# Kernel tuning notes

Hardware: AMD Instinct MI355X
Metric: run time of the kernel (lower is better)

Reference implementation:

```python
import jax, jax.numpy as jnp
import numpy as np
from jax import lax

G, BS = 8, 32  # group_num, blocksize


def conv(x, w, b=None, stride=1, pad=0):
    out = lax.conv_general_dilated(x, w, (stride, stride), [(pad, pad), (pad, pad)],
                                   dimension_numbers=('NCHW', 'OIHW', 'NCHW'))
    if b is not None:
        out = out + b[None, :, None, None]
    return out


def prelu(x, a):
    return jnp.where(x >= 0, x, a * x)


def reshape_adap(x, bs):
    # faithful vectorized form of My_Reshape_Adap: channel c = co*bs*bs + p*bs + q
    # goes to output[b, co, i*bs+p, j*bs+q]
    B, C, h, w = x.shape
    co = C // (bs * bs)
    return x.reshape(B, co, bs, bs, h, w).transpose(0, 1, 4, 2, 5, 3).reshape(B, co, h * bs, w * bs)


def setup_inputs() -> dict:
    key = jax.random.key(0)
    ks = jax.random.split(key, 24)
    rn = lambda k, shp, s: (jax.random.normal(k, shp, dtype=jnp.float32) * s)
    inp = {
        'x': rn(ks[0], (1, 1, 256, 256), 1.0),
        'sample_w': rn(ks[1], (G, 13, 1, 32, 32), 0.03),
        'up_w': rn(ks[2], (G, 1024, 13, 1, 1), 0.2),
        'up_b': rn(ks[3], (G, 1024), 0.02),
        'h1_w': rn(ks[4], (G, 64, 1, 3, 3), 0.2),
        'h1_b': rn(ks[5], (G, 64), 0.02),
        'h1_a': jnp.full((G,), 0.25, jnp.float32),
        'fus_w': rn(ks[6], (G - 1, 64, 128, 3, 3), 0.03),
        'fus_b': rn(ks[7], (G - 1, 64), 0.02),
        'fus_a': jnp.full((G - 1,), 0.25, jnp.float32),
        't2_w': rn(ks[8], (G, 64, 64, 3, 3), 0.04),
        't2_b': rn(ks[9], (G, 64), 0.02),
        't2_a': jnp.full((G,), 0.25, jnp.float32),
        't3_w': rn(ks[10], (G, 64, 64, 3, 3), 0.04),
        't3_b': rn(ks[11], (G, 64), 0.02),
        't3_a': jnp.full((G,), 0.25, jnp.float32),
        't4_w': rn(ks[12], (G, 64, 64, 3, 3), 0.04),
        't4_b': rn(ks[13], (G, 64), 0.02),
        't4_a': jnp.full((G,), 0.25, jnp.float32),
        't5_w': rn(ks[14], (G, 1, 64, 3, 3), 0.04),
        't5_b': rn(ks[15], (G, 1), 0.02),
    }
    return inp


def reference(x, sample_w, up_w, up_b, h1_w, h1_b, h1_a, fus_w, fus_b, fus_a,
              t2_w, t2_b, t2_a, t3_w, t3_b, t3_a, t4_w, t4_b, t4_a, t5_w, t5_b):
    outs = []
    feature = None
    for m in range(G):
        # SamplingModule: conv(1->13, k=32, s=32, no bias)
        s = conv(x, sample_w[m], stride=BS)
        # HeadBlock: 1x1 upsample (13->1024) + block scatter reshape + conv(1->64)+PReLU
        u = conv(s, up_w[m], up_b[m])
        r = reshape_adap(u, BS)                       # [B,1,H,W]
        h = prelu(conv(r, h1_w[m], h1_b[m], pad=1), h1_a[m])  # [B,64,H,W]
        if m == 0:
            feature = h
        else:
            # Fusion_concate: conv(128->64)+PReLU on channel concat
            cat = jnp.concatenate([feature, h], axis=1)
            feature = prelu(conv(cat, fus_w[m - 1], fus_b[m - 1], pad=1), fus_a[m - 1])
        t = prelu(conv(feature, t2_w[m], t2_b[m], pad=1), t2_a[m])
        t = prelu(conv(t, t3_w[m], t3_b[m], pad=1), t3_a[m])
        t = prelu(conv(t, t4_w[m], t4_b[m], pad=1), t4_a[m])
        outs.append(conv(t, t5_w[m], t5_b[m], pad=1))
    return jnp.stack(outs)  # [G, B, 1, H, W]
```

## Files before the change

### kernel.cpp

```cpp
#include <hip/hip_runtime.h>

constexpr int H = 256, W = 256, NPIX = H * W;
constexpr int PW = 258;
constexpr size_t PLANE = (size_t)PW * PW * 64;

typedef _Float16 half8 __attribute__((ext_vector_type(8)));
typedef _Float16 half4 __attribute__((ext_vector_type(4)));
typedef float    f32x4 __attribute__((ext_vector_type(4)));
typedef float    f32x16 __attribute__((ext_vector_type(16)));

__device__ __forceinline__ void gl16(const _Float16* g, _Float16* l)
{
    __builtin_amdgcn_global_load_lds(
        (const __attribute__((address_space(1))) unsigned int*)g,
        (__attribute__((address_space(3))) unsigned int*)l, 16, 0, 0);
}

__global__ __launch_bounds__(256)
void prep_k(const float* __restrict__ x, const float* __restrict__ sw,
            const float* __restrict__ uw, const float* __restrict__ ub,
            const float* __restrict__ t2w, const float* __restrict__ t3w,
            const float* __restrict__ t4w, const float* __restrict__ fusw,
            _Float16* __restrict__ planes, _Float16* __restrict__ w16,
            float* __restrict__ r_all)
{
    const int b = blockIdx.x, t = threadIdx.x;
    for (int idx = b * 256 + t; idx < 24 * 1028 * 8; idx += 512 * 256) {
        int c = idx & 7, rem = idx >> 3;
        int p = rem / 1028, bb = rem % 1028;
        int gy, gx;
        if (bb < 258)      { gy = 0;            gx = bb; }
        else if (bb < 516) { gy = 257;          gx = bb - 258; }
        else if (bb < 772) { gy = bb - 516 + 1; gx = 0; }
        else               { gy = bb - 772 + 1; gx = 257; }
        f32x4 z = {0.f, 0.f, 0.f, 0.f};
        *(f32x4*)(planes + (size_t)p * PLANE + ((size_t)(gy * PW + gx) * 64) + c * 8) = z;
    }
    for (int idx = b * 256 + t; idx < 38 * 36864; idx += 512 * 256) {
        int blk = idx / 36864, r2 = idx % 36864;
        int e = r2 & 7, co = (r2 >> 3) & 63, hh = (r2 >> 9) & 1, kk = (r2 >> 10) & 3,
            tap = r2 >> 12;
        const float* src; int cin, cib;
        if (blk < 24) {
            int which = blk >> 3, m = blk & 7;
            src = (which == 0 ? t2w : which == 1 ? t3w : t4w) + (size_t)m * 64 * 64 * 9;
            cin = 64; cib = 0;
        } else {
            int f = (blk - 24) >> 1; cib = ((blk - 24) & 1) * 64;
            src = fusw + (size_t)f * 64 * 128 * 9; cin = 128;
        }
        int ci = cib + (kk * 2 + hh) * 8 + e;
        w16[idx] = (_Float16)src[((size_t)co * cin + ci) * 9 + tap];
    }
    {
        int m = b >> 6, ij = b & 63;
        int i = ij >> 3, j = ij & 7;
        __shared__ float s_lds[16];
        if (t < 208) {
            int c = t >> 4, sub = t & 15;
            float acc = 0.f;
            for (int k = sub * 64; k < sub * 64 + 64; ++k) {
                int p = k >> 5, q = k & 31;
                acc += x[(i * 32 + p) * W + (j * 32 + q)] * sw[(m * 13 + c) * 1024 + k];
            }
            #pragma unroll
            for (int off = 8; off; off >>= 1) acc += __shfl_down(acc, off, 16);
            if (sub == 0) s_lds[c] = acc;
        }
        __syncthreads();
        const float* uwm = uw + m * 1024 * 13;
        float* rm = r_all + m * NPIX;
        #pragma unroll
        for (int pi = 0; pi < 4; ++pi) {
            int px = pi * 256 + t;
            int p = px >> 5, q = px & 31;
            int oc = p * 32 + q;
            float acc = ub[m * 1024 + oc];
            #pragma unroll
            for (int c = 0; c < 13; ++c) acc = fmaf(uwm[oc * 13 + c], s_lds[c], acc);
            rm[((i * 32 + p) << 8) + j * 32 + q] = acc;
        }
    }
}

__global__ __launch_bounds__(256)
void h1_k(const float* __restrict__ r_all, const float* __restrict__ w,
          const float* __restrict__ b, const float* __restrict__ a,
          _Float16* __restrict__ f0)
{
    const float* r = r_all;
    const int t = threadIdx.x;
    const int px = t & 63, cog = t >> 6;
    const int y = blockIdx.x >> 2;
    const int x = ((blockIdx.x & 3) << 6) + px;
    float v[9];
    #pragma unroll
    for (int dy = 0; dy < 3; ++dy) {
        int gy = y + dy - 1;
        #pragma unroll
        for (int dx = 0; dx < 3; ++dx) {
            int gx = x + dx - 1;
            v[dy*3+dx] = ((unsigned)gy < 256u && (unsigned)gx < 256u)
                       ? r[(gy << 8) + gx] : 0.f;
        }
    }
    const float slope = a[0];
    _Float16* op = f0 + ((size_t)((y + 1) * PW + (x + 1))) * 64 + cog * 16;
    #pragma unroll
    for (int cg2 = 0; cg2 < 2; ++cg2) {
        half8 o;
        #pragma unroll
        for (int j = 0; j < 8; ++j) {
            int co = cog * 16 + cg2 * 8 + j;
            float acc = b[co];
            #pragma unroll
            for (int k = 0; k < 9; ++k) acc = fmaf(v[k], w[co*9+k], acc);
            acc = acc >= 0.f ? acc : slope * acc;
            o[j] = (_Float16)acc;
        }
        *(half8*)(op + cg2 * 8) = o;
    }
}

__global__ __launch_bounds__(128, 2)
void conv_mfma_k(const _Float16* __restrict__ in0, const _Float16* __restrict__ w0,
                 const float* __restrict__ bias, const float* __restrict__ alpha,
                 _Float16* __restrict__ out)
{
    const int t    = threadIdx.x;
    const int lane = t & 63;
    const int wv   = t >> 6;
    const int b    = blockIdx.x;
    const int m    = b >> 7;
    const int rem  = b & 127;
    const int xq   = rem & 3;
    const int y0   = (rem >> 2) << 3;
    const int x0   = xq << 6;

    const _Float16* inp0 = in0 + (size_t)m * PLANE;
    _Float16*       outp = out + (size_t)m * PLANE;
    const _Float16* wp0  = w0 + (size_t)m * 36864;
    const float*    bp   = bias + m * 64;
    const float     slope = alpha[m];

    const int h = lane >> 5, cl = lane & 31;
    const int cobase = wv * 32;

    extern __shared__ __align__(16) char smem[];
    _Float16* li = (_Float16*)smem;

    half8 Areg[36];
    #pragma unroll
    for (int tap = 0; tap < 9; ++tap)
        #pragma unroll
        for (int kk = 0; kk < 4; ++kk)
            Areg[tap*4+kk] = *(const half8*)(wp0 +
                (size_t)(((tap*4+kk)*2 + h)*64 + cobase + cl) * 8);

    auto stage_row = [&](int pr) {
        const int slot = pr & 3;
        #pragma unroll
        for (int i = 0; i < 5; ++i) {
            int f = i * 128 + t;
            if (i < 4 || f < 528) {
                int hx = f >> 3, c = f & 7;
                gl16(inp0 + ((size_t)(pr * PW + x0 + hx) * 64 + (c ^ (hx & 7)) * 8),
                     li + (size_t)(slot * 528 + f) * 8);
            }
        }
    };

    f32x16 acc0, acc1;

    stage_row(y0); stage_row(y0 + 1); stage_row(y0 + 2);
    __syncthreads();
    #pragma unroll 1
    for (int s = 0; s < 8; ++s) {
        if (s < 7) stage_row(y0 + s + 3);
        #pragma unroll
        for (int q = 0; q < 4; ++q)
            #pragma unroll
            for (int j = 0; j < 4; ++j) {
                float bb = bp[cobase + q * 8 + 4 * h + j];
                acc0[q*4+j] = bb; acc1[q*4+j] = bb;
            }
        __builtin_amdgcn_s_setprio(1);
        #pragma unroll
        for (int tap = 0; tap < 9; ++tap) {
            const int dy = tap / 3, dx = tap % 3;
            const int slot = (y0 + s + dy) & 3;
            const int hx0 = cl + dx;
            const int hx1 = hx0 + 32;
            const int sw8 = hx0 & 7;
            #pragma unroll
            for (int kk = 0; kk < 4; ++kk) {
                const int c = kk * 2 + h;
                half8 b0 = *(const half8*)(li + ((size_t)(slot*528 + hx0*8 + (c ^ sw8))) * 8);
                half8 b1 = *(const half8*)(li + ((size_t)(slot*528 + hx1*8 + (c ^ sw8))) * 8);
                acc0 = __builtin_amdgcn_mfma_f32_32x32x16_f16(Areg[tap*4+kk], b0, acc0, 0, 0, 0);
                acc1 = __builtin_amdgcn_mfma_f32_32x32x16_f16(Areg[tap*4+kk], b1, acc1, 0, 0, 0);
            }
        }
        __builtin_amdgcn_s_setprio(0);
        const int y = y0 + s;
        #pragma unroll
        for (int pt = 0; pt < 2; ++pt) {
            const size_t gp = (size_t)((y + 1) * PW + (x0 + pt * 32 + cl + 1)) * 64;
            const f32x16& A0 = pt ? acc1 : acc0;
            #pragma unroll
            for (int q = 0; q < 4; ++q) {
                half4 v0;
                #pragma unroll
                for (int j = 0; j < 4; ++j) {
                    float xv = A0[q*4+j];
                    xv = xv >= 0.f ? xv : slope * xv;
                    v0[j] = (_Float16)v0[j];
                    v0[j] = (_Float16)xv;
                }
                *(half4*)(outp + gp + cobase + q * 8 + 4 * h) = v0;
            }
        }
        if (s < 7) {
            asm volatile("s_waitcnt vmcnt(8)" ::: "memory");
            __builtin_amdgcn_s_barrier();
            __builtin_amdgcn_sched_barrier(0);
        }
    }
}

__global__ __launch_bounds__(256, 2)
void fus_k(const _Float16* __restrict__ fprev, const float* __restrict__ rm,
           const float* __restrict__ h1w, const float* __restrict__ h1b,
           const float* __restrict__ h1a,
           const _Float16* __restrict__ wf, const _Float16* __restrict__ wh,
           const float* __restrict__ bias, const float* __restrict__ alpha,
           _Float16* __restrict__ outp)
{
    const int t = threadIdx.x, lane = t & 63, wv = t >> 6;
    const int b = blockIdx.x;
    const int xcd = b & 7, u = b >> 3, xq = u & 3, band = u >> 2;
    const int y0 = xcd * 32 + band * 2, x0 = xq * 64;
    const int h = lane >> 5, cl = lane & 31;
    const int px0 = (wv & 1) * 32, cobase = (wv >> 1) * 32;

    __shared__ __align__(16) _Float16 ringF[4 * 528 * 8];
    __shared__ __align__(16) _Float16 ringH[4 * 528 * 8];

    #pragma unroll
    for (int i = 0; i < 9; ++i) {
        int idx = i * 256 + t;
        if (i < 8 || idx < 2112) {
            int r = idx / 528, f = idx - r * 528;
            int hx = f >> 3, c = f & 7;
            gl16(fprev + ((size_t)((y0 + r) * PW + x0 + hx) * 64 + (c ^ (hx & 7)) * 8),
                 ringF + (size_t)idx * 8);
        }
    }
    {
        const int c8 = t & 7;
        float wreg[72];
        #pragma unroll
        for (int i = 0; i < 18; ++i)
            *(f32x4*)(wreg + i * 4) = *(const f32x4*)(h1w + c8 * 72 + i * 4);
        float b8[8];
        #pragma unroll
        for (int j = 0; j < 8; ++j) b8[j] = h1b[c8 * 8 + j];
        const float hs = h1a[0];

        #pragma unroll
        for (int it = 0; it < 9; ++it) {
            int idx = it * 256 + t;
            if (it < 8 || idx < 2112) {
                int pl = idx >> 3;
                int r  = pl / 66, hx = pl - r * 66;
                int gy = y0 - 1 + r, gx = x0 - 1 + hx;
                half8 o = {0,0,0,0,0,0,0,0};
                if ((unsigned)gy < 256u && (unsigned)gx < 256u) {
                    float v[9];
                    #pragma unroll
                    for (int dy = 0; dy < 3; ++dy) {
                        int ry = gy + dy - 1;
                        #pragma unroll
                        for (int dx = 0; dx < 3; ++dx) {
                            int rx = gx + dx - 1;
                            v[dy*3+dx] = ((unsigned)ry < 256u && (unsigned)rx < 256u)
                                       ? rm[(ry << 8) + rx] : 0.f;
                        }
                    }
                    #pragma unroll
                    for (int j = 0; j < 8; ++j) {
                        float av = b8[j];
                        #pragma unroll
                        for (int k = 0; k < 9; ++k) av = fmaf(v[k], wreg[j*9+k], av);
                        av = av >= 0.f ? av : hs * av;
                        o[j] = (_Float16)av;
                    }
                }
                *(half8*)(ringH + (size_t)(r * 528 + hx * 8 + (c8 ^ (hx & 7))) * 8) = o;
            }
        }
    }
    __builtin_amdgcn_sched_barrier(0);

    half8 Areg[36];
    auto load_A = [&](const _Float16* w) {
        #pragma unroll
        for (int tap = 0; tap < 9; ++tap)
            #pragma unroll
            for (int kk = 0; kk < 4; ++kk)
                Areg[tap*4+kk] = *(const half8*)(w +
                    (size_t)(((tap*4+kk)*2 + h)*64 + cobase + cl) * 8);
    };
    load_A(wf);

    f32x16 acc0, acc1;
    #pragma unroll
    for (int q = 0; q < 4; ++q)
        #pragma unroll
        for (int j = 0; j < 4; ++j) {
            float bb = bias[cobase + q * 8 + 4 * h + j];
            acc0[q*4+j] = bb; acc1[q*4+j] = bb;
        }

    __syncthreads();

    auto cpass = [&](const _Float16* ring) {
        __builtin_amdgcn_s_setprio(1);
        #pragma unroll
        for (int tap = 0; tap < 9; ++tap) {
            const int dy = tap / 3, dx = tap % 3;
            const int hx = px0 + cl + dx;
            const int sw = hx & 7;
            #pragma unroll
            for (int kk = 0; kk < 4; ++kk) {
                const int c = kk * 2 + h;
                half8 b0 = *(const half8*)(ring + ((size_t)(((dy    )*528) + hx*8 + (c ^ sw))) * 8);
                half8 b1 = *(const half8*)(ring + ((size_t)(((dy + 1)*528) + hx*8 + (c ^ sw))) * 8);
                acc0 = __builtin_amdgcn_mfma_f32_32x32x16_f16(Areg[tap*4+kk], b0, acc0, 0, 0, 0);
                acc1 = __builtin_amdgcn_mfma_f32_32x32x16_f16(Areg[tap*4+kk], b1, acc1, 0, 0, 0);
            }
        }
        __builtin_amdgcn_s_setprio(0);
    };

    cpass(ringF);
    load_A(wh);
    cpass(ringH);

    const float slope = alpha[0];
    #pragma unroll
    for (int s = 0; s < 2; ++s) {
        const size_t gp = (size_t)((y0 + s + 1) * PW + (x0 + px0 + cl + 1)) * 64 + cobase;
        const f32x16& A0 = s ? acc1 : acc0;
        #pragma unroll
        for (int q = 0; q < 4; ++q) {
            half4 v;
            #pragma unroll
            for (int j = 0; j < 4; ++j) {
                float xv = A0[q*4+j];
                xv = xv >= 0.f ? xv : slope * xv;
                v[j] = (_Float16)xv;
            }
            *(half4*)(outp + gp + q * 8 + 4 * h) = v;
        }
    }
}

__global__ __launch_bounds__(256, 2)
void t5_k(const _Float16* __restrict__ in_all, const float* __restrict__ w_all,
          const float* __restrict__ b_all, float* __restrict__ out_all)
{
    const int m = blockIdx.y;
    const _Float16* in = in_all + (size_t)m * PLANE;
    const float* w = w_all + m * 576;
    float* outp = out_all + m * NPIX;

    const int t = threadIdx.x;
    const int b = blockIdx.x;
    const int xcd = b & 7, u = b >> 3;
    const int xh = u & 1, band = u >> 1;
    const int y0 = xcd * 32 + band * 8;
    const int x0 = xh << 7;

    __shared__ __align__(16) _Float16 ring[4 * 130 * 64];
    __shared__ float wl[576];
    __shared__ float part[128];

    auto stage_row = [&](int pr) {
        const int slot = pr & 3;
        #pragma unroll
        for (int i = 0; i < 5; ++i) {
            int f = i * 256 + t;
            if (i < 4 || f < 1040) {
                int hx = f >> 3, c = f & 7;
                gl16(in + ((size_t)(pr * PW + x0 + hx) * 64 + (c ^ (hx & 7)) * 8),
                     ring + (size_t)(slot * 1040 + f) * 8);
            }
        }
    };

    stage_row(y0); stage_row(y0 + 1); stage_row(y0 + 2);
    #pragma unroll
    for (int i = 0; i < 3; ++i) { int idx = i*256 + t; if (idx < 576) wl[idx] = w[idx]; }
    __syncthreads();

    const int p = t & 127, chalf = t >> 7;
    #pragma unroll 1
    for (int s = 0; s < 8; ++s) {
        if (s < 7) stage_row(y0 + s + 3);
        float acc = 0.f;
        #pragma unroll
        for (int dy = 0; dy < 3; ++dy) {
            const int slot = (y0 + s + dy) & 3;
            #pragma unroll
            for (int dx = 0; dx < 3; ++dx) {
                const int hx = p + dx, sw = hx & 7, tap = dy * 3 + dx;
                #pragma unroll
                for (int kc = 0; kc < 4; ++kc) {
                    const int c8 = chalf * 4 + kc;
                    half8 vv = *(const half8*)(ring +
                        ((size_t)((slot*130 + hx)*8 + (c8 ^ sw))) * 8);
                    #pragma unroll
                    for (int e = 0; e < 8; ++e)
                        acc = fmaf((float)vv[e], wl[(c8 * 8 + e) * 9 + tap], acc);
                }
            }
        }
        if (chalf) part[p] = acc;
        __syncthreads();
        if (!chalf) outp[((y0 + s) << 8) + x0 + p] = part[p] + acc + b_all[m];
        __syncthreads();
    }
}

extern "C" void kernel_launch(void* const* d_in, const int* in_sizes, int n_in,
                              void* d_out, int out_size, void* d_ws, size_t ws_size,
                              hipStream_t stream)
{
    const float* x        = (const float*)d_in[0];
    const float* sample_w = (const float*)d_in[1];
    const float* up_w     = (const float*)d_in[2];
    const float* up_b     = (const float*)d_in[3];
    const float* h1_w     = (const float*)d_in[4];
    const float* h1_b     = (const float*)d_in[5];
    const float* h1_a     = (const float*)d_in[6];
    const float* fus_w    = (const float*)d_in[7];
    const float* fus_b    = (const float*)d_in[8];
    const float* fus_a    = (const float*)d_in[9];
    const float* t2_w     = (const float*)d_in[10];
    const float* t2_b     = (const float*)d_in[11];
    const float* t2_a     = (const float*)d_in[12];
    const float* t3_w     = (const float*)d_in[13];
    const float* t3_b     = (const float*)d_in[14];
    const float* t3_a     = (const float*)d_in[15];
    const float* t4_w     = (const float*)d_in[16];
    const float* t4_b     = (const float*)d_in[17];
    const float* t4_a     = (const float*)d_in[18];
    const float* t5_w     = (const float*)d_in[19];
    const float* t5_b     = (const float*)d_in[20];

    float* out = (float*)d_out;
    char*  wsb = (char*)d_ws;

    _Float16* w16    = (_Float16*)wsb;
    float*    r_all  = (float*)(wsb + 2801664);
    _Float16* f_all  = (_Float16*)(wsb + 4898816);
    _Float16* sc_all = f_all + 8 * PLANE;
    _Float16* t1_all = sc_all + 8 * PLANE;

    auto wblk = [&](int b) { return w16 + (size_t)b * 36864; };

    prep_k<<<512, 256, 0, stream>>>(x, sample_w, up_w, up_b,
                                    t2_w, t3_w, t4_w, fus_w,
                                    f_all, w16, r_all);
    h1_k<<<1024, 256, 0, stream>>>(r_all, h1_w, h1_b, h1_a, f_all);

    for (int m = 1; m < 8; ++m) {
        fus_k<<<512, 256, 0, stream>>>(
            f_all + (size_t)(m - 1) * PLANE,
            r_all + m * NPIX, h1_w + m * 576, h1_b + m * 64, h1_a + m,
            wblk(24 + (m - 1) * 2), wblk(24 + (m - 1) * 2 + 1),
            fus_b + (m - 1) * 64, fus_a + (m - 1),
            f_all + (size_t)m * PLANE);
    }

    const size_t LDSB = 33792;
    conv_mfma_k<<<1024, 128, LDSB, stream>>>(f_all, wblk(0), t2_b, t2_a, t1_all);
    conv_mfma_k<<<1024, 128, LDSB, stream>>>(t1_all, wblk(8), t3_b, t3_a, sc_all);
    conv_mfma_k<<<1024, 128, LDSB, stream>>>(sc_all, wblk(16), t4_b, t4_a, t1_all);
    t5_k<<<dim3(64, 8), 256, 0, stream>>>(t1_all, t5_w, t5_b, out);
}
```

Baseline: 393.2 us.

## Widen conv tile to 128 pixels per block and stage h1 input in LDS

The tail conv kernel now runs 256-thread blocks that each cover a 128-pixel-wide row strip, with four waves split across pixel halves and output-channel halves. This halves the block count, and the halo columns are shared by twice as many pixels, so less input is reloaded from global memory. LDS use per block roughly doubles, which may limit how many blocks fit per CU. Separately, the fusion kernel loads its r-map neighbourhood once into a small shared tile instead of doing nine bounds-checked global reads per pixel.

Result: faster. 361.7 us (-8.0%).

```diff
diff --git a/kernel.cpp b/kernel.cpp
--- a/kernel.cpp
+++ b/kernel.cpp
@@ -122,7 +122,7 @@
     }
 }
 
-__global__ __launch_bounds__(128, 2)
+__global__ __launch_bounds__(256, 2)
 void conv_mfma_k(const _Float16* __restrict__ in0, const _Float16* __restrict__ w0,
                  const float* __restrict__ bias, const float* __restrict__ alpha,
                  _Float16* __restrict__ out)
@@ -131,20 +131,20 @@
     const int lane = t & 63;
     const int wv   = t >> 6;
     const int b    = blockIdx.x;
-    const int m    = b >> 7;
-    const int rem  = b & 127;
-    const int xq   = rem & 3;
-    const int y0   = (rem >> 2) << 3;
-    const int x0   = xq << 6;
+    const int m    = b >> 6;
+    const int rem  = b & 63;
+    const int xh   = rem & 1;
+    const int y0   = (rem >> 1) << 3;
 
     const _Float16* inp0 = in0 + (size_t)m * PLANE;
     _Float16*       outp = out + (size_t)m * PLANE;
     const _Float16* wp0  = w0 + (size_t)m * 36864;
     const float*    bp   = bias + m * 64;
     const float     slope = alpha[m];
+    const int x0 = xh << 7;
 
     const int h = lane >> 5, cl = lane & 31;
-    const int cobase = wv * 32;
+    const int px0 = (wv & 1) * 64, cobase = (wv >> 1) * 32;
 
     extern __shared__ __align__(16) char smem[];
     _Float16* li = (_Float16*)smem;
@@ -161,11 +161,11 @@
         const int slot = pr & 3;
         #pragma unroll
         for (int i = 0; i < 5; ++i) {
-            int f = i * 128 + t;
-            if (i < 4 || f < 528) {
+            int f = i * 256 + t;
+            if (i < 4 || f < 1040) {
                 int hx = f >> 3, c = f & 7;
                 gl16(inp0 + ((size_t)(pr * PW + x0 + hx) * 64 + (c ^ (hx & 7)) * 8),
-                     li + (size_t)(slot * 528 + f) * 8);
+                     li + (size_t)(slot * 1040 + f) * 8);
             }
         }
     };
@@ -189,14 +189,14 @@
         for (int tap = 0; tap < 9; ++tap) {
             const int dy = tap / 3, dx = tap % 3;
             const int slot = (y0 + s + dy) & 3;
-            const int hx0 = cl + dx;
+            const int hx0 = px0 + cl + dx;
             const int hx1 = hx0 + 32;
             const int sw8 = hx0 & 7;
             #pragma unroll
             for (int kk = 0; kk < 4; ++kk) {
                 const int c = kk * 2 + h;
-                half8 b0 = *(const half8*)(li + ((size_t)(slot*528 + hx0*8 + (c ^ sw8))) * 8);
-                half8 b1 = *(const half8*)(li + ((size_t)(slot*528 + hx1*8 + (c ^ sw8))) * 8);
+                half8 b0 = *(const half8*)(li + ((size_t)((slot*130 + hx0)*8 + (c ^ sw8))) * 8);
+                half8 b1 = *(const half8*)(li + ((size_t)((slot*130 + hx1)*8 + (c ^ sw8))) * 8);
                 acc0 = __builtin_amdgcn_mfma_f32_32x32x16_f16(Areg[tap*4+kk], b0, acc0, 0, 0, 0);
                 acc1 = __builtin_amdgcn_mfma_f32_32x32x16_f16(Areg[tap*4+kk], b1, acc1, 0, 0, 0);
             }
@@ -205,7 +205,7 @@
         const int y = y0 + s;
         #pragma unroll
         for (int pt = 0; pt < 2; ++pt) {
-            const size_t gp = (size_t)((y + 1) * PW + (x0 + pt * 32 + cl + 1)) * 64;
+            const size_t gp = (size_t)((y + 1) * PW + (x0 + px0 + pt * 32 + cl + 1)) * 64;
             const f32x16& A0 = pt ? acc1 : acc0;
             #pragma unroll
             for (int q = 0; q < 4; ++q) {
@@ -214,7 +214,6 @@
                 for (int j = 0; j < 4; ++j) {
                     float xv = A0[q*4+j];
                     xv = xv >= 0.f ? xv : slope * xv;
-                    v0[j] = (_Float16)v0[j];
                     v0[j] = (_Float16)xv;
                 }
                 *(half4*)(outp + gp + cobase + q * 8 + 4 * h) = v0;
@@ -245,6 +244,7 @@
 
     __shared__ __align__(16) _Float16 ringF[4 * 528 * 8];
     __shared__ __align__(16) _Float16 ringH[4 * 528 * 8];
+    __shared__ float rtile[6 * 68];
 
     #pragma unroll
     for (int i = 0; i < 9; ++i) {
@@ -256,6 +256,21 @@
                  ringF + (size_t)idx * 8);
         }
     }
+
+    #pragma unroll
+    for (int i = 0; i < 2; ++i) {
+        int ix = i * 256 + t;
+        if (ix < 408) {
+            int row = ix / 68, col = ix - row * 68;
+            int gy = y0 - 2 + row, gx = x0 - 2 + col;
+            rtile[ix] = ((unsigned)gy < 256u && (unsigned)gx < 256u)
+                      ? rm[(gy << 8) + gx] : 0.f;
+        }
+    }
+    asm volatile("s_waitcnt lgkmcnt(0)" ::: "memory");
+    __builtin_amdgcn_s_barrier();
+    __builtin_amdgcn_sched_barrier(0);
+
     {
         const int c8 = t & 7;
         float wreg[72];
@@ -278,15 +293,10 @@
                 if ((unsigned)gy < 256u && (unsigned)gx < 256u) {
                     float v[9];
                     #pragma unroll
-                    for (int dy = 0; dy < 3; ++dy) {
-                        int ry = gy + dy - 1;
+                    for (int dy = 0; dy < 3; ++dy)
                         #pragma unroll
-                        for (int dx = 0; dx < 3; ++dx) {
-                            int rx = gx + dx - 1;
-                            v[dy*3+dx] = ((unsigned)ry < 256u && (unsigned)rx < 256u)
-                                       ? rm[(ry << 8) + rx] : 0.f;
-                        }
-                    }
+                        for (int dx = 0; dx < 3; ++dx)
+                            v[dy*3+dx] = rtile[(r + dy) * 68 + hx + dx];
                     #pragma unroll
                     for (int j = 0; j < 8; ++j) {
                         float av = b8[j];
@@ -484,9 +494,9 @@
             f_all + (size_t)m * PLANE);
     }
 
-    const size_t LDSB = 33792;
-    conv_mfma_k<<<1024, 128, LDSB, stream>>>(f_all, wblk(0), t2_b, t2_a, t1_all);
-    conv_mfma_k<<<1024, 128, LDSB, stream>>>(t1_all, wblk(8), t3_b, t3_a, sc_all);
-    conv_mfma_k<<<1024, 128, LDSB, stream>>>(sc_all, wblk(16), t4_b, t4_a, t1_all);
+    const size_t LDSB = 66560;
+    conv_mfma_k<<<512, 256, LDSB, stream>>>(f_all, wblk(0), t2_b, t2_a, t1_all);
+    conv_mfma_k<<<512, 256, LDSB, stream>>>(t1_all, wblk(8), t3_b, t3_a, sc_all);
+    conv_mfma_k<<<512, 256, LDSB, stream>>>(sc_all, wblk(16), t4_b, t4_a, t1_all);
     t5_k<<<dim3(64, 8), 256, 0, stream>>>(t1_all, t5_w, t5_b, out);
 }
```
